# Performance work log

Measured on AMD Instinct MI355X. Metric: run time of the kernel, lower is better.

The kernel has to match this reference:

```python
import jax, jax.numpy as jnp
import numpy as np

K_NN = 2       # module k: number of nearest neighbors used for mean kNN distance
ALPHA = 1.1    # threshold = mean + alpha * std


def setup_inputs() -> dict:
    key = jax.random.key(0)
    x = jax.random.normal(key, (16, 4096, 3), dtype=jnp.float32)
    return {"x": x}


def reference(x):
    # x: [B, K, 3] point cloud
    # pairwise squared distances: ||xi||^2 - 2 xi.xj + ||xj||^2  -> [B, K, K]
    inner = -2.0 * jnp.einsum("bkd,bjd->bkj", x, x)
    xx = jnp.sum(x * x, axis=-1)                       # [B, K]
    dist = xx[:, :, None] + inner + xx[:, None, :]     # [B, K, K]

    # k+1 smallest distances (includes self-distance 0), drop self
    neg_value, _ = jax.lax.top_k(-dist, K_NN + 1)      # [B, K, k+1]
    value = -neg_value[..., 1:]                        # [B, K, k] kNN distances
    value = jnp.mean(value, axis=-1)                   # [B, K] mean kNN distance

    mean = jnp.mean(value, axis=-1)                    # [B]
    std = jnp.std(value, axis=-1, ddof=1)              # [B] unbiased, like torch.std
    threshold = mean + ALPHA * std                     # [B]
    bool_mask = value <= threshold[:, None]            # [B, K]

    # Original returns a ragged list x[i][mask[i]]; for fixed shapes under jit we
    # return the points with outliers zeroed plus the boolean keep-mask, which
    # carries identical information.
    sel_pc = jnp.where(bool_mask[..., None], x, jnp.zeros((), x.dtype))  # [B, K, 3]
    return sel_pc, bool_mask
```

## Files before the change

kernel.cpp:

```cpp
#include <hip/hip_runtime.h>
#include <math.h>

#define B_SZ 16
#define K_PTS 4096
#define ALPHA 1.1f

#define JS 8
#define JT (K_PTS / JS)
#define ICH 1024
#define IPT 4
#define THR 256

#define BIGF 3.0e38f

__device__ __forceinline__ void insert3(float d, float& m0, float& m1, float& m2) {
    m2 = __builtin_amdgcn_fmed3f(d, m1, m2);
    m1 = __builtin_amdgcn_fmed3f(d, m0, m1);
    m0 = fminf(d, m0);
}

__global__ __launch_bounds__(256) void sor_partial(
    const float* __restrict__ x, float* __restrict__ ws)
{
    __shared__ float4 pts[JT];
    const int b  = blockIdx.y;
    const int js = blockIdx.x & (JS - 1);
    const int ic = blockIdx.x / JS;
    const int j0 = js * JT;
    const float* xb = x + (size_t)b * K_PTS * 3;

    for (int p = threadIdx.x; p < JT; p += THR) {
        float a0 = xb[(j0 + p) * 3 + 0];
        float a1 = xb[(j0 + p) * 3 + 1];
        float a2 = xb[(j0 + p) * 3 + 2];
        pts[p] = make_float4(a0, a1, a2, a0 * a0 + a1 * a1 + a2 * a2);
    }
    __syncthreads();

    const int ibase = ic * ICH + threadIdx.x;
    float x2[IPT], y2[IPT], z2[IPT];
    float m0[IPT], m1[IPT], m2[IPT];
    #pragma unroll
    for (int k = 0; k < IPT; ++k) {
        const int i = ibase + k * THR;
        x2[k] = -2.0f * xb[i * 3 + 0];
        y2[k] = -2.0f * xb[i * 3 + 1];
        z2[k] = -2.0f * xb[i * 3 + 2];
        m0[k] = BIGF; m1[k] = BIGF; m2[k] = BIGF;
    }

    #pragma unroll 4
    for (int j = 0; j < JT; ++j) {
        const float4 pj = pts[j];
        #pragma unroll
        for (int k = 0; k < IPT; ++k) {
            float t = fmaf(z2[k], pj.z, pj.w);
            t = fmaf(y2[k], pj.y, t);
            float d = fmaf(x2[k], pj.x, t);
            insert3(d, m0[k], m1[k], m2[k]);
        }
    }

    #pragma unroll
    for (int k = 0; k < IPT; ++k) {
        const int i = ibase + k * THR;
        float* w = ws + (size_t)((b * JS + js) * 3) * K_PTS + i;
        w[0]          = m0[k];
        w[K_PTS]      = m1[k];
        w[2 * K_PTS]  = m2[k];
    }
}

__global__ __launch_bounds__(256) void sor_merge(
    const float* __restrict__ x, const float* __restrict__ ws,
    float* __restrict__ value)
{
    const int gid = blockIdx.x * 256 + threadIdx.x;
    const int b = gid >> 12;
    const int i = gid & (K_PTS - 1);

    float m0 = BIGF, m1 = BIGF, m2 = BIGF;
    #pragma unroll
    for (int js = 0; js < JS; ++js) {
        #pragma unroll
        for (int s = 0; s < 3; ++s) {
            float d = ws[(size_t)((b * JS + js) * 3 + s) * K_PTS + i];
            insert3(d, m0, m1, m2);
        }
    }
    const float a0 = x[(size_t)gid * 3 + 0];
    const float a1 = x[(size_t)gid * 3 + 1];
    const float a2 = x[(size_t)gid * 3 + 2];
    const float xx = a0 * a0 + a1 * a1 + a2 * a2;
    value[gid] = ((m1 + xx) + (m2 + xx)) * 0.5f;
}

__global__ __launch_bounds__(1024) void sor_mask_kernel(
    const float* __restrict__ x, float* __restrict__ out)
{
    const int b = blockIdx.x;
    const int tid = threadIdx.x;
    float* value = out + (size_t)B_SZ * K_PTS * 3;
    float* selpc = out;

    __shared__ float red[16];
    __shared__ float sh_mean, sh_thr;

    float v[4];
    float s = 0.0f;
    #pragma unroll
    for (int k = 0; k < 4; ++k) {
        v[k] = value[b * K_PTS + tid + k * 1024];
        s += v[k];
    }
    #pragma unroll
    for (int off = 32; off > 0; off >>= 1) s += __shfl_down(s, off, 64);
    if ((tid & 63) == 0) red[tid >> 6] = s;
    __syncthreads();
    if (tid == 0) {
        float t = 0.0f;
        for (int w = 0; w < 16; ++w) t += red[w];
        sh_mean = t * (1.0f / (float)K_PTS);
    }
    __syncthreads();
    const float mean = sh_mean;

    float q = 0.0f;
    #pragma unroll
    for (int k = 0; k < 4; ++k) { float dv = v[k] - mean; q += dv * dv; }
    #pragma unroll
    for (int off = 32; off > 0; off >>= 1) q += __shfl_down(q, off, 64);
    if ((tid & 63) == 0) red[tid >> 6] = q;
    __syncthreads();
    if (tid == 0) {
        float t = 0.0f;
        for (int w = 0; w < 16; ++w) t += red[w];
        sh_thr = mean + ALPHA * sqrtf(t / (float)(K_PTS - 1));
    }
    __syncthreads();
    const float thr = sh_thr;

    #pragma unroll
    for (int k = 0; k < 4; ++k) {
        const int i = tid + k * 1024;
        const bool keep = v[k] <= thr;
        value[b * K_PTS + i] = keep ? 1.0f : 0.0f;
        const size_t base = ((size_t)b * K_PTS + i) * 3;
        float x0 = x[base + 0];
        float x1 = x[base + 1];
        float x2 = x[base + 2];
        selpc[base + 0] = keep ? x0 : 0.0f;
        selpc[base + 1] = keep ? x1 : 0.0f;
        selpc[base + 2] = keep ? x2 : 0.0f;
    }
}

__global__ __launch_bounds__(256) void sor_value_kernel(
    const float* __restrict__ x, float* __restrict__ value)
{
    __shared__ float4 pts[K_PTS];
    const int b = blockIdx.y;
    const float* xb = x + (size_t)b * K_PTS * 3;
    for (int p = threadIdx.x; p < K_PTS; p += 256) {
        float a0 = xb[p * 3 + 0];
        float a1 = xb[p * 3 + 1];
        float a2 = xb[p * 3 + 2];
        pts[p] = make_float4(a0, a1, a2, a0 * a0 + a1 * a1 + a2 * a2);
    }
    __syncthreads();
    const int i = blockIdx.x * 256 + threadIdx.x;
    const float4 pi = pts[i];
    float m0 = BIGF, m1 = BIGF, m2 = BIGF;
    #pragma unroll 8
    for (int j = 0; j < K_PTS; ++j) {
        float4 pj = pts[j];
        float dot = pi.x * pj.x + pi.y * pj.y + pi.z * pj.z;
        float d = (pi.w - 2.0f * dot) + pj.w;
        insert3(d, m0, m1, m2);
    }
    value[b * K_PTS + i] = 0.5f * (m1 + m2);
}

extern "C" void kernel_launch(void* const* d_in, const int* in_sizes, int n_in,
                              void* d_out, int out_size, void* d_ws, size_t ws_size,
                              hipStream_t stream)
{
    const float* x = (const float*)d_in[0];
    float* out = (float*)d_out;
    float* value = out + (size_t)B_SZ * K_PTS * 3;
    const size_t ws_needed = (size_t)B_SZ * JS * 3 * K_PTS * sizeof(float);

    if (ws_size >= ws_needed) {
        float* ws = (float*)d_ws;
        dim3 gA((K_PTS / ICH) * JS, B_SZ);
        sor_partial<<<gA, THR, 0, stream>>>(x, ws);
        sor_merge<<<(B_SZ * K_PTS) / 256, 256, 0, stream>>>(x, ws, value);
    } else {
        dim3 g1(K_PTS / 256, B_SZ);
        sor_value_kernel<<<g1, 256, 0, stream>>>(x, value);
    }
    sor_mask_kernel<<<B_SZ, 1024, 0, stream>>>(x, out);
}
```

Before: 51.88 us.

## Drop self-distance in diagonal blocks, keep top-2 only, fuse merge into mask kernel

Only the diagonal j-block that contains point i now tracks top-3, and it drops the self-distance before writing. All other blocks track just the two smallest distances, so the workspace shrinks from three candidates per split to two. The j-split doubles from 8 to 16 to give the partial kernel more blocks. The separate merge kernel is folded into the mask kernel, which removes one launch and the round trip of value through global memory. The cost is that the merge-and-mask stage now runs on only 16 blocks and reads 32 candidates per point. It also relies on the self-distance being the minimum in its own block, which assumes there are no duplicate points.

```diff
diff --git a/kernel.cpp b/kernel.cpp
--- a/kernel.cpp
+++ b/kernel.cpp
@@ -5,31 +5,35 @@
 #define K_PTS 4096
 #define ALPHA 1.1f
 
-#define JS 8
-#define JT (K_PTS / JS)
+#define JS 16
+#define JTT (K_PTS / JS)
 #define ICH 1024
 #define IPT 4
 #define THR 256
 
 #define BIGF 3.0e38f
 
+__device__ __forceinline__ void insert2(float d, float& m0, float& m1) {
+    m1 = __builtin_amdgcn_fmed3f(d, m0, m1);
+    m0 = fminf(d, m0);
+}
 __device__ __forceinline__ void insert3(float d, float& m0, float& m1, float& m2) {
     m2 = __builtin_amdgcn_fmed3f(d, m1, m2);
     m1 = __builtin_amdgcn_fmed3f(d, m0, m1);
     m0 = fminf(d, m0);
 }
 
-__global__ __launch_bounds__(256) void sor_partial(
+__global__ __launch_bounds__(256) void sor_partial2(
     const float* __restrict__ x, float* __restrict__ ws)
 {
-    __shared__ float4 pts[JT];
+    __shared__ float4 pts[JTT];
     const int b  = blockIdx.y;
-    const int js = blockIdx.x & (JS - 1);
-    const int ic = blockIdx.x / JS;
-    const int j0 = js * JT;
+    const int ic = blockIdx.x >> 4;
+    const int js = blockIdx.x & 15;
+    const int j0 = js * JTT;
     const float* xb = x + (size_t)b * K_PTS * 3;
 
-    for (int p = threadIdx.x; p < JT; p += THR) {
+    for (int p = threadIdx.x; p < JTT; p += THR) {
         float a0 = xb[(j0 + p) * 3 + 0];
         float a1 = xb[(j0 + p) * 3 + 1];
         float a2 = xb[(j0 + p) * 3 + 2];
@@ -38,81 +42,99 @@
     __syncthreads();
 
     const int ibase = ic * ICH + threadIdx.x;
-    float x2[IPT], y2[IPT], z2[IPT];
-    float m0[IPT], m1[IPT], m2[IPT];
+    float x2[IPT], y2[IPT], z2[IPT], m0[IPT], m1[IPT];
     #pragma unroll
     for (int k = 0; k < IPT; ++k) {
         const int i = ibase + k * THR;
         x2[k] = -2.0f * xb[i * 3 + 0];
         y2[k] = -2.0f * xb[i * 3 + 1];
         z2[k] = -2.0f * xb[i * 3 + 2];
-        m0[k] = BIGF; m1[k] = BIGF; m2[k] = BIGF;
-    }
-
-    #pragma unroll 4
-    for (int j = 0; j < JT; ++j) {
-        const float4 pj = pts[j];
+        m0[k] = BIGF; m1[k] = BIGF;
+    }
+
+    float* wbase = ws + (size_t)((b * JS + js) * 2) * K_PTS;
+
+    if ((js >> 2) == ic) {
+        float m2[IPT];
+        #pragma unroll
+        for (int k = 0; k < IPT; ++k) m2[k] = BIGF;
+
+        #pragma unroll 4
+        for (int j = 0; j < JTT; ++j) {
+            const float4 pj = pts[j];
+            #pragma unroll
+            for (int k = 0; k < IPT; ++k) {
+                float t = fmaf(z2[k], pj.z, pj.w);
+                t = fmaf(y2[k], pj.y, t);
+                float d = fmaf(x2[k], pj.x, t);
+                insert3(d, m0[k], m1[k], m2[k]);
+            }
+        }
+        const int kstar = js & 3;
         #pragma unroll
         for (int k = 0; k < IPT; ++k) {
-            float t = fmaf(z2[k], pj.z, pj.w);
-            t = fmaf(y2[k], pj.y, t);
-            float d = fmaf(x2[k], pj.x, t);
-            insert3(d, m0[k], m1[k], m2[k]);
-        }
-    }
-
-    #pragma unroll
-    for (int k = 0; k < IPT; ++k) {
-        const int i = ibase + k * THR;
-        float* w = ws + (size_t)((b * JS + js) * 3) * K_PTS + i;
-        w[0]          = m0[k];
-        w[K_PTS]      = m1[k];
-        w[2 * K_PTS]  = m2[k];
-    }
-}
-
-__global__ __launch_bounds__(256) void sor_merge(
+            const int i = ibase + k * THR;
+            const bool drop0 = (k == kstar);
+            wbase[i]         = drop0 ? m1[k] : m0[k];
+            wbase[K_PTS + i] = drop0 ? m2[k] : m1[k];
+        }
+    } else {
+        #pragma unroll 4
+        for (int j = 0; j < JTT; ++j) {
+            const float4 pj = pts[j];
+            #pragma unroll
+            for (int k = 0; k < IPT; ++k) {
+                float t = fmaf(z2[k], pj.z, pj.w);
+                t = fmaf(y2[k], pj.y, t);
+                float d = fmaf(x2[k], pj.x, t);
+                insert2(d, m0[k], m1[k]);
+            }
+        }
+        #pragma unroll
+        for (int k = 0; k < IPT; ++k) {
+            const int i = ibase + k * THR;
+            wbase[i]         = m0[k];
+            wbase[K_PTS + i] = m1[k];
+        }
+    }
+}
+
+__global__ __launch_bounds__(1024) void sor_merge_mask(
     const float* __restrict__ x, const float* __restrict__ ws,
-    float* __restrict__ value)
-{
-    const int gid = blockIdx.x * 256 + threadIdx.x;
-    const int b = gid >> 12;
-    const int i = gid & (K_PTS - 1);
-
-    float m0 = BIGF, m1 = BIGF, m2 = BIGF;
-    #pragma unroll
-    for (int js = 0; js < JS; ++js) {
-        #pragma unroll
-        for (int s = 0; s < 3; ++s) {
-            float d = ws[(size_t)((b * JS + js) * 3 + s) * K_PTS + i];
-            insert3(d, m0, m1, m2);
-        }
-    }
-    const float a0 = x[(size_t)gid * 3 + 0];
-    const float a1 = x[(size_t)gid * 3 + 1];
-    const float a2 = x[(size_t)gid * 3 + 2];
-    const float xx = a0 * a0 + a1 * a1 + a2 * a2;
-    value[gid] = ((m1 + xx) + (m2 + xx)) * 0.5f;
-}
-
-__global__ __launch_bounds__(1024) void sor_mask_kernel(
-    const float* __restrict__ x, float* __restrict__ out)
+    float* __restrict__ out)
 {
     const int b = blockIdx.x;
     const int tid = threadIdx.x;
-    float* value = out + (size_t)B_SZ * K_PTS * 3;
+    float* maskout = out + (size_t)B_SZ * K_PTS * 3;
     float* selpc = out;
 
     __shared__ float red[16];
     __shared__ float sh_mean, sh_thr;
 
     float v[4];
+    #pragma unroll
+    for (int k = 0; k < 4; ++k) {
+        const int i = tid + k * 1024;
+        float m0 = BIGF, m1 = BIGF;
+        #pragma unroll
+        for (int js = 0; js < JS; ++js) {
+            const float* w = ws + (size_t)((b * JS + js) * 2) * K_PTS + i;
+            float d0 = w[0];
+            float d1 = w[K_PTS];
+            insert2(d0, m0, m1);
+            insert2(d1, m0, m1);
+        }
+        const size_t base = ((size_t)b * K_PTS + i) * 3;
+        const float a0 = x[base + 0];
+        const float a1 = x[base + 1];
+        const float a2 = x[base + 2];
+        const float xx = a0 * a0 + a1 * a1 + a2 * a2;
+        v[k] = ((m0 + xx) + (m1 + xx)) * 0.5f;
+    }
+
     float s = 0.0f;
     #pragma unroll
-    for (int k = 0; k < 4; ++k) {
-        v[k] = value[b * K_PTS + tid + k * 1024];
-        s += v[k];
-    }
+    for (int k = 0; k < 4; ++k) s += v[k];
     #pragma unroll
     for (int off = 32; off > 0; off >>= 1) s += __shfl_down(s, off, 64);
     if ((tid & 63) == 0) red[tid >> 6] = s;
@@ -144,7 +166,7 @@
     for (int k = 0; k < 4; ++k) {
         const int i = tid + k * 1024;
         const bool keep = v[k] <= thr;
-        value[b * K_PTS + i] = keep ? 1.0f : 0.0f;
+        maskout[b * K_PTS + i] = keep ? 1.0f : 0.0f;
         const size_t base = ((size_t)b * K_PTS + i) * 3;
         float x0 = x[base + 0];
         float x1 = x[base + 1];
@@ -153,6 +175,12 @@
         selpc[base + 1] = keep ? x1 : 0.0f;
         selpc[base + 2] = keep ? x2 : 0.0f;
     }
+}
+
+__device__ __forceinline__ void insert3f(float d, float& m0, float& m1, float& m2) {
+    m2 = __builtin_amdgcn_fmed3f(d, m1, m2);
+    m1 = __builtin_amdgcn_fmed3f(d, m0, m1);
+    m0 = fminf(d, m0);
 }
 
 __global__ __launch_bounds__(256) void sor_value_kernel(
@@ -176,9 +204,52 @@
         float4 pj = pts[j];
         float dot = pi.x * pj.x + pi.y * pj.y + pi.z * pj.z;
         float d = (pi.w - 2.0f * dot) + pj.w;
-        insert3(d, m0, m1, m2);
+        insert3f(d, m0, m1, m2);
     }
     value[b * K_PTS + i] = 0.5f * (m1 + m2);
+}
+
+__global__ __launch_bounds__(1024) void sor_mask_kernel(
+    const float* __restrict__ x, float* __restrict__ out)
+{
+    const int b = blockIdx.x;
+    const int tid = threadIdx.x;
+    float* value = out + (size_t)B_SZ * K_PTS * 3;
+    float* selpc = out;
+    __shared__ float red[16];
+    __shared__ float sh_mean, sh_thr;
+    float v[4];
+    float s = 0.0f;
+    #pragma unroll
+    for (int k = 0; k < 4; ++k) { v[k] = value[b * K_PTS + tid + k * 1024]; s += v[k]; }
+    #pragma unroll
+    for (int off = 32; off > 0; off >>= 1) s += __shfl_down(s, off, 64);
+    if ((tid & 63) == 0) red[tid >> 6] = s;
+    __syncthreads();
+    if (tid == 0) { float t = 0.0f; for (int w = 0; w < 16; ++w) t += red[w]; sh_mean = t / (float)K_PTS; }
+    __syncthreads();
+    const float mean = sh_mean;
+    float q = 0.0f;
+    #pragma unroll
+    for (int k = 0; k < 4; ++k) { float dv = v[k] - mean; q += dv * dv; }
+    #pragma unroll
+    for (int off = 32; off > 0; off >>= 1) q += __shfl_down(q, off, 64);
+    if ((tid & 63) == 0) red[tid >> 6] = q;
+    __syncthreads();
+    if (tid == 0) { float t = 0.0f; for (int w = 0; w < 16; ++w) t += red[w]; sh_thr = mean + ALPHA * sqrtf(t / (float)(K_PTS - 1)); }
+    __syncthreads();
+    const float thr = sh_thr;
+    #pragma unroll
+    for (int k = 0; k < 4; ++k) {
+        const int i = tid + k * 1024;
+        const bool keep = v[k] <= thr;
+        value[b * K_PTS + i] = keep ? 1.0f : 0.0f;
+        const size_t base = ((size_t)b * K_PTS + i) * 3;
+        float x0 = x[base + 0]; float x1 = x[base + 1]; float x2 = x[base + 2];
+        selpc[base + 0] = keep ? x0 : 0.0f;
+        selpc[base + 1] = keep ? x1 : 0.0f;
+        selpc[base + 2] = keep ? x2 : 0.0f;
+    }
 }
 
 extern "C" void kernel_launch(void* const* d_in, const int* in_sizes, int n_in,
@@ -187,17 +258,18 @@
 {
     const float* x = (const float*)d_in[0];
     float* out = (float*)d_out;
-    float* value = out + (size_t)B_SZ * K_PTS * 3;
-    const size_t ws_needed = (size_t)B_SZ * JS * 3 * K_PTS * sizeof(float);
+
+    const size_t ws_needed = (size_t)B_SZ * JS * 2 * K_PTS * sizeof(float);
 
     if (ws_size >= ws_needed) {
         float* ws = (float*)d_ws;
         dim3 gA((K_PTS / ICH) * JS, B_SZ);
-        sor_partial<<<gA, THR, 0, stream>>>(x, ws);
-        sor_merge<<<(B_SZ * K_PTS) / 256, 256, 0, stream>>>(x, ws, value);
+        sor_partial2<<<gA, THR, 0, stream>>>(x, ws);
+        sor_merge_mask<<<B_SZ, 1024, 0, stream>>>(x, ws, out);
     } else {
+        float* value = out + (size_t)B_SZ * K_PTS * 3;
         dim3 g1(K_PTS / 256, B_SZ);
         sor_value_kernel<<<g1, 256, 0, stream>>>(x, value);
-    }
-    sor_mask_kernel<<<B_SZ, 1024, 0, stream>>>(x, out);
-}
+        sor_mask_kernel<<<B_SZ, 1024, 0, stream>>>(x, out);
+    }
+}
```

New measurement: 53.06 us. 2.3% more time.

## Exclude self-distance structurally to track top-2 instead of top-3 per chunk

Applied to the files above, without the earlier changes.

Splits the neighbor range into 16 chunks and identifies the single chunk per thread slot that contains the point itself. Only that slot keeps three minima and drops the self-distance; all others track just two minima. This cuts one median op per pair and shrinks workspace traffic in the merge, while doubling the grid for more parallelism. It adds a divergent diagonal branch and relies on the self-distance being the chunk minimum.

```diff
diff --git a/kernel.cpp b/kernel.cpp
--- a/kernel.cpp
+++ b/kernel.cpp
@@ -5,31 +5,34 @@
 #define K_PTS 4096
 #define ALPHA 1.1f
 
-#define JS 8
-#define JT (K_PTS / JS)
+#define JS 16
+#define JTT (K_PTS / JS)
 #define ICH 1024
-#define IPT 4
 #define THR 256
 
 #define BIGF 3.0e38f
 
+__device__ __forceinline__ void insert2(float d, float& m0, float& m1) {
+    m1 = __builtin_amdgcn_fmed3f(d, m0, m1);
+    m0 = fminf(d, m0);
+}
 __device__ __forceinline__ void insert3(float d, float& m0, float& m1, float& m2) {
     m2 = __builtin_amdgcn_fmed3f(d, m1, m2);
     m1 = __builtin_amdgcn_fmed3f(d, m0, m1);
     m0 = fminf(d, m0);
 }
 
-__global__ __launch_bounds__(256) void sor_partial(
+__global__ __launch_bounds__(256) void sor_partial2(
     const float* __restrict__ x, float* __restrict__ ws)
 {
-    __shared__ float4 pts[JT];
+    __shared__ float4 pts[JTT];
     const int b  = blockIdx.y;
-    const int js = blockIdx.x & (JS - 1);
-    const int ic = blockIdx.x / JS;
-    const int j0 = js * JT;
+    const int ic = blockIdx.x >> 4;
+    const int js = blockIdx.x & 15;
+    const int j0 = js * JTT;
     const float* xb = x + (size_t)b * K_PTS * 3;
 
-    for (int p = threadIdx.x; p < JT; p += THR) {
+    for (int p = threadIdx.x; p < JTT; p += THR) {
         float a0 = xb[(j0 + p) * 3 + 0];
         float a1 = xb[(j0 + p) * 3 + 1];
         float a2 = xb[(j0 + p) * 3 + 2];
@@ -38,36 +41,69 @@
     __syncthreads();
 
     const int ibase = ic * ICH + threadIdx.x;
-    float x2[IPT], y2[IPT], z2[IPT];
-    float m0[IPT], m1[IPT], m2[IPT];
-    #pragma unroll
-    for (int k = 0; k < IPT; ++k) {
-        const int i = ibase + k * THR;
-        x2[k] = -2.0f * xb[i * 3 + 0];
-        y2[k] = -2.0f * xb[i * 3 + 1];
-        z2[k] = -2.0f * xb[i * 3 + 2];
-        m0[k] = BIGF; m1[k] = BIGF; m2[k] = BIGF;
-    }
-
-    #pragma unroll 4
-    for (int j = 0; j < JT; ++j) {
-        const float4 pj = pts[j];
+    const bool diag = ((js >> 2) == ic);
+    const int kstar = js & 3;
+
+    int idx[4];
+    #pragma unroll
+    for (int c = 0; c < 4; ++c) idx[c] = ibase + c * THR;
+    if (diag) { idx[0] = ibase + kstar * THR; idx[kstar] = ibase; }
+
+    float x2[4], y2[4], z2[4], m0[4], m1[4];
+    #pragma unroll
+    for (int c = 0; c < 4; ++c) {
+        const float* p = xb + (size_t)idx[c] * 3;
+        x2[c] = -2.0f * p[0];
+        y2[c] = -2.0f * p[1];
+        z2[c] = -2.0f * p[2];
+        m0[c] = BIGF; m1[c] = BIGF;
+    }
+
+    float* wbase = ws + (size_t)((b * JS + js) * 2) * K_PTS;
+
+    if (diag) {
+        float m2_0 = BIGF;
+        #pragma unroll 8
+        for (int j = 0; j < JTT; ++j) {
+            const float4 pj = pts[j];
+            {
+                float t = fmaf(z2[0], pj.z, pj.w);
+                t = fmaf(y2[0], pj.y, t);
+                float d = fmaf(x2[0], pj.x, t);
+                insert3(d, m0[0], m1[0], m2_0);
+            }
+            #pragma unroll
+            for (int c = 1; c < 4; ++c) {
+                float t = fmaf(z2[c], pj.z, pj.w);
+                t = fmaf(y2[c], pj.y, t);
+                float d = fmaf(x2[c], pj.x, t);
+                insert2(d, m0[c], m1[c]);
+            }
+        }
+        wbase[idx[0]]         = m1[0];
+        wbase[K_PTS + idx[0]] = m2_0;
         #pragma unroll
-        for (int k = 0; k < IPT; ++k) {
-            float t = fmaf(z2[k], pj.z, pj.w);
-            t = fmaf(y2[k], pj.y, t);
-            float d = fmaf(x2[k], pj.x, t);
-            insert3(d, m0[k], m1[k], m2[k]);
-        }
-    }
-
-    #pragma unroll
-    for (int k = 0; k < IPT; ++k) {
-        const int i = ibase + k * THR;
-        float* w = ws + (size_t)((b * JS + js) * 3) * K_PTS + i;
-        w[0]          = m0[k];
-        w[K_PTS]      = m1[k];
-        w[2 * K_PTS]  = m2[k];
+        for (int c = 1; c < 4; ++c) {
+            wbase[idx[c]]         = m0[c];
+            wbase[K_PTS + idx[c]] = m1[c];
+        }
+    } else {
+        #pragma unroll 8
+        for (int j = 0; j < JTT; ++j) {
+            const float4 pj = pts[j];
+            #pragma unroll
+            for (int c = 0; c < 4; ++c) {
+                float t = fmaf(z2[c], pj.z, pj.w);
+                t = fmaf(y2[c], pj.y, t);
+                float d = fmaf(x2[c], pj.x, t);
+                insert2(d, m0[c], m1[c]);
+            }
+        }
+        #pragma unroll
+        for (int c = 0; c < 4; ++c) {
+            wbase[idx[c]]         = m0[c];
+            wbase[K_PTS + idx[c]] = m1[c];
+        }
     }
 }
 
@@ -79,20 +115,18 @@
     const int b = gid >> 12;
     const int i = gid & (K_PTS - 1);
 
-    float m0 = BIGF, m1 = BIGF, m2 = BIGF;
+    float m0 = BIGF, m1 = BIGF;
     #pragma unroll
     for (int js = 0; js < JS; ++js) {
-        #pragma unroll
-        for (int s = 0; s < 3; ++s) {
-            float d = ws[(size_t)((b * JS + js) * 3 + s) * K_PTS + i];
-            insert3(d, m0, m1, m2);
-        }
+        const float* w = ws + (size_t)((b * JS + js) * 2) * K_PTS + i;
+        insert2(w[0], m0, m1);
+        insert2(w[K_PTS], m0, m1);
     }
     const float a0 = x[(size_t)gid * 3 + 0];
     const float a1 = x[(size_t)gid * 3 + 1];
     const float a2 = x[(size_t)gid * 3 + 2];
     const float xx = a0 * a0 + a1 * a1 + a2 * a2;
-    value[gid] = ((m1 + xx) + (m2 + xx)) * 0.5f;
+    value[gid] = ((m0 + xx) + (m1 + xx)) * 0.5f;
 }
 
 __global__ __launch_bounds__(1024) void sor_mask_kernel(
@@ -188,12 +222,13 @@
     const float* x = (const float*)d_in[0];
     float* out = (float*)d_out;
     float* value = out + (size_t)B_SZ * K_PTS * 3;
-    const size_t ws_needed = (size_t)B_SZ * JS * 3 * K_PTS * sizeof(float);
+
+    const size_t ws_needed = (size_t)B_SZ * JS * 2 * K_PTS * sizeof(float);
 
     if (ws_size >= ws_needed) {
         float* ws = (float*)d_ws;
         dim3 gA((K_PTS / ICH) * JS, B_SZ);
-        sor_partial<<<gA, THR, 0, stream>>>(x, ws);
+        sor_partial2<<<gA, THR, 0, stream>>>(x, ws);
         sor_merge<<<(B_SZ * K_PTS) / 256, 256, 0, stream>>>(x, ws, value);
     } else {
         dim3 g1(K_PTS / 256, B_SZ);
```

Result: faster. 45.33 us, median of 2 (-12.6%).
